# Performance work log

Measured on AMD Instinct MI355X. Metric: run time of the kernel, lower is better.

## Reference

```python
import jax, jax.numpy as jnp
import numpy as np

N_NODES = 100000
N_EDGES = 1000000
D_IN, H1, H2, D_OUT = 64, 64, 32, 16


def gcn_conv(x, W, b, src, dst, n):
    # PyG GCNConv: add self-loops, symmetric normalization deg^-1/2 A deg^-1/2, then linear.
    h = x @ W  # [N, out]
    ones = jnp.ones(src.shape[0], dtype=x.dtype)
    deg = jax.ops.segment_sum(ones, dst, num_segments=n) + 1.0  # +1 for self-loop
    dinv = jnp.where(deg > 0, jax.lax.rsqrt(deg), 0.0)
    coef = dinv[src] * dinv[dst]  # [E]
    msg = h[src] * coef[:, None]  # [E, out]
    agg = jax.ops.segment_sum(msg, dst, num_segments=n)
    agg = agg + h * (dinv * dinv)[:, None]  # self-loop contribution
    return agg + b


def setup_inputs() -> dict:
    key = jax.random.key(0)
    ks = jax.random.split(key, 16)
    s = 0.1
    inp = {
        "x": jax.random.normal(ks[0], (N_NODES, D_IN), jnp.float32),
        "edge_index": jax.random.randint(ks[1], (2, N_EDGES), 0, N_NODES, jnp.int64),
        # SELayer params
        "U_w": jax.random.normal(ks[2], (D_IN, D_IN), jnp.float32) * s,
        "U_b": jnp.zeros((D_IN,), jnp.float32),
        "fc1_w": jax.random.normal(ks[3], (D_IN, D_IN // 4), jnp.float32) * s,
        "fc1_b": jnp.zeros((D_IN // 4,), jnp.float32),
        "fc2_w": jax.random.normal(ks[4], (D_IN // 4, D_IN), jnp.float32) * s,
        "fc2_b": jnp.zeros((D_IN,), jnp.float32),
        # GCN layers
        "W1": jax.random.normal(ks[5], (D_IN, H1), jnp.float32) * s,
        "b1": jnp.zeros((H1,), jnp.float32),
        "W2": jax.random.normal(ks[6], (H1, H2), jnp.float32) * s,
        "b2": jnp.zeros((H2,), jnp.float32),
        # classifier
        "fc_w": jax.random.normal(ks[7], (H2, D_OUT), jnp.float32) * s,
        "fc_b": jnp.zeros((D_OUT,), jnp.float32),
    }
    return inp


def reference(x, edge_index, U_w, U_b, fc1_w, fc1_b, fc2_w, fc2_b, W1, b1, W2, b2, fc_w, fc_b):
    n = x.shape[0]
    src, dst = edge_index[0], edge_index[1]
    # SE layer
    xu = x @ U_w + U_b
    w = jax.nn.sigmoid(jax.nn.relu(xu @ fc1_w + fc1_b) @ fc2_w + fc2_b)
    h = xu * w
    # GCN stack (dropout is identity in eval mode)
    h = jax.nn.relu(gcn_conv(h, W1, b1, src, dst, n))
    h = jax.nn.relu(gcn_conv(h, W2, b2, src, dst, n))
    logits = h @ fc_w + fc_b
    return jax.nn.log_softmax(logits, axis=1), w
```

## Files before the change

kernel.cpp:

```cpp
#include <hip/hip_runtime.h>
#include <hip/hip_bf16.h>

#define NN 100000
#define NE 1000000
#define CAP 64
#define PADS 16

#define NPER 196
#define GRID_FAT (NPER * 13)

__device__ __forceinline__ float f4c(const float4& v, int i) {
    switch (i) { case 0: return v.x; case 1: return v.y; case 2: return v.z; default: return v.w; }
}
__device__ __forceinline__ unsigned short f2bf(float f) {
    unsigned u = __float_as_uint(f);
    return (unsigned short)((u + 0x7FFFu + ((u >> 16) & 1u)) >> 16);
}
__device__ __forceinline__ float bf2f(unsigned short s) {
    return __uint_as_float(((unsigned)s) << 16);
}

__global__ __launch_bounds__(256) void fat_kernel(
    const float* __restrict__ x, const void* __restrict__ eidx,
    const float* __restrict__ U_w, const float* __restrict__ U_b,
    const float* __restrict__ f1w, const float* __restrict__ f1b,
    const float* __restrict__ f2w, const float* __restrict__ f2b,
    const float* __restrict__ W1,
    int* __restrict__ cnt_pad, int* __restrict__ bucket,
    unsigned short* __restrict__ hW1b, float* __restrict__ w_out)
{
    const int b = blockIdx.x;
    const int r13 = b % 13;
    const int tid = threadIdx.x;

    if (r13 < 5) {
        const int sidx = (b / 13) * 5 + r13;
        long e0 = ((long)sidx * 256 + tid) * 4;
        if (e0 >= NE) return;

        const unsigned* pp = (const unsigned*)eidx;
        bool is64 = true;
#pragma unroll
        for (int k = 0; k < 8; ++k)
            if (pp[2 * k + 1] != 0u) is64 = false;

        int srcs[4], dsts[4];
        if (is64) {
            const long long* p = (const long long*)eidx;
#pragma unroll
            for (int i = 0; i < 4; ++i) {
                srcs[i] = (int)p[e0 + i];
                dsts[i] = (int)p[NE + e0 + i];
            }
        } else {
            const int* p = (const int*)eidx;
            int4 s4 = *(const int4*)&p[e0];
            int4 d4 = *(const int4*)&p[NE + e0];
            srcs[0] = s4.x; srcs[1] = s4.y; srcs[2] = s4.z; srcs[3] = s4.w;
            dsts[0] = d4.x; dsts[1] = d4.y; dsts[2] = d4.z; dsts[3] = d4.w;
        }

        int pos[4];
#pragma unroll
        for (int i = 0; i < 4; ++i) pos[i] = atomicAdd(&cnt_pad[dsts[i] * PADS], 1);
#pragma unroll
        for (int i = 0; i < 4; ++i)
            if (pos[i] < CAP) bucket[dsts[i] * CAP + pos[i]] = srcs[i];
        return;
    }

    const int seidx = (b / 13) * 8 + (r13 - 5);
    const long base = (long)seidx * 64;
    if (base >= NN) return;

    __shared__ float sU[64][68];
    __shared__ float sx[64][68];
    __shared__ float sF1[64 * 16];
    __shared__ float st1[64][20];
    __shared__ float sF2[16][68];
    __shared__ float sUb[64], sb1[16], sb2[64];

    for (int i = tid; i < 1024; i += 256) {
        int r = i >> 4, q = i & 15;
        *(float4*)&sU[r][q * 4] = *(const float4*)&U_w[r * 64 + q * 4];
    }
    for (int i = tid; i < 1024; i += 256) {
        int r = i >> 4, q = i & 15;
        long row = base + r;
        float4 v = make_float4(0.f, 0.f, 0.f, 0.f);
        if (row < NN) v = *(const float4*)&x[row * 64 + q * 4];
        *(float4*)&sx[r][q * 4] = v;
    }
    for (int i = tid; i < 1024; i += 256) sF1[i] = f1w[i];
    {
        int r = tid >> 4, q = tid & 15;
        *(float4*)&sF2[r][q * 4] = *(const float4*)&f2w[r * 64 + q * 4];
    }
    if (tid < 64) sUb[tid] = U_b[tid];
    if (tid < 16) sb1[tid] = f1b[tid];
    if (tid < 64) sb2[tid] = f2b[tid];
    __syncthreads();

    const int cg = tid & 15, rg = tid >> 4;
    const int r0 = rg * 4, c0 = cg * 4;

    float acc[4][4];
#pragma unroll
    for (int ri = 0; ri < 4; ++ri)
#pragma unroll
        for (int ci = 0; ci < 4; ++ci) acc[ri][ci] = 0.f;

#pragma unroll 4
    for (int kk = 0; kk < 64; kk += 4) {
        float4 xa[4];
#pragma unroll
        for (int ri = 0; ri < 4; ++ri) xa[ri] = *(float4*)&sx[r0 + ri][kk];
#pragma unroll
        for (int kq = 0; kq < 4; ++kq) {
            float4 ub = *(float4*)&sU[kk + kq][c0];
#pragma unroll
            for (int ri = 0; ri < 4; ++ri) {
                float xv = f4c(xa[ri], kq);
                acc[ri][0] = fmaf(xv, ub.x, acc[ri][0]);
                acc[ri][1] = fmaf(xv, ub.y, acc[ri][1]);
                acc[ri][2] = fmaf(xv, ub.z, acc[ri][2]);
                acc[ri][3] = fmaf(xv, ub.w, acc[ri][3]);
            }
        }
    }
    __syncthreads();

#pragma unroll
    for (int ri = 0; ri < 4; ++ri) {
        acc[ri][0] += sUb[c0 + 0];
        acc[ri][1] += sUb[c0 + 1];
        acc[ri][2] += sUb[c0 + 2];
        acc[ri][3] += sUb[c0 + 3];
        float4 o = make_float4(acc[ri][0], acc[ri][1], acc[ri][2], acc[ri][3]);
        *(float4*)&sx[r0 + ri][c0] = o;
    }
    __syncthreads();

    float a1[4] = {sb1[cg], sb1[cg], sb1[cg], sb1[cg]};
#pragma unroll 4
    for (int kk = 0; kk < 64; kk += 4) {
        float4 xa[4];
#pragma unroll
        for (int ri = 0; ri < 4; ++ri) xa[ri] = *(float4*)&sx[r0 + ri][kk];
#pragma unroll
        for (int kq = 0; kq < 4; ++kq) {
            float wv = sF1[(kk + kq) * 16 + cg];
#pragma unroll
            for (int ri = 0; ri < 4; ++ri) a1[ri] = fmaf(f4c(xa[ri], kq), wv, a1[ri]);
        }
    }
#pragma unroll
    for (int ri = 0; ri < 4; ++ri) st1[r0 + ri][cg] = fmaxf(a1[ri], 0.f);
    __syncthreads();

    float a2[4][4];
#pragma unroll
    for (int ri = 0; ri < 4; ++ri)
#pragma unroll
        for (int ci = 0; ci < 4; ++ci) a2[ri][ci] = sb2[c0 + ci];

#pragma unroll
    for (int kk = 0; kk < 16; kk += 4) {
        float4 ta[4];
#pragma unroll
        for (int ri = 0; ri < 4; ++ri) ta[ri] = *(float4*)&st1[r0 + ri][kk];
#pragma unroll
        for (int kq = 0; kq < 4; ++kq) {
            float4 fb = *(float4*)&sF2[kk + kq][c0];
#pragma unroll
            for (int ri = 0; ri < 4; ++ri) {
                float xv = f4c(ta[ri], kq);
                a2[ri][0] = fmaf(xv, fb.x, a2[ri][0]);
                a2[ri][1] = fmaf(xv, fb.y, a2[ri][1]);
                a2[ri][2] = fmaf(xv, fb.z, a2[ri][2]);
                a2[ri][3] = fmaf(xv, fb.w, a2[ri][3]);
            }
        }
    }
#pragma unroll
    for (int ri = 0; ri < 4; ++ri) {
        long row = base + r0 + ri;
        float4 wv;
        wv.x = 1.f / (1.f + expf(-a2[ri][0]));
        wv.y = 1.f / (1.f + expf(-a2[ri][1]));
        wv.z = 1.f / (1.f + expf(-a2[ri][2]));
        wv.w = 1.f / (1.f + expf(-a2[ri][3]));
        float4 h4;
        h4.x = acc[ri][0] * wv.x; h4.y = acc[ri][1] * wv.y;
        h4.z = acc[ri][2] * wv.z; h4.w = acc[ri][3] * wv.w;
        *(float4*)&sx[r0 + ri][c0] = h4;
        if (row < NN) *(float4*)&w_out[row * 64 + c0] = wv;
    }
    for (int i = tid; i < 1024; i += 256) {
        int r = i >> 4, q = i & 15;
        *(float4*)&sU[r][q * 4] = *(const float4*)&W1[r * 64 + q * 4];
    }
    __syncthreads();

#pragma unroll
    for (int ri = 0; ri < 4; ++ri)
#pragma unroll
        for (int ci = 0; ci < 4; ++ci) acc[ri][ci] = 0.f;

#pragma unroll 4
    for (int kk = 0; kk < 64; kk += 4) {
        float4 xa[4];
#pragma unroll
        for (int ri = 0; ri < 4; ++ri) xa[ri] = *(float4*)&sx[r0 + ri][kk];
#pragma unroll
        for (int kq = 0; kq < 4; ++kq) {
            float4 wb = *(float4*)&sU[kk + kq][c0];
#pragma unroll
            for (int ri = 0; ri < 4; ++ri) {
                float xv = f4c(xa[ri], kq);
                acc[ri][0] = fmaf(xv, wb.x, acc[ri][0]);
                acc[ri][1] = fmaf(xv, wb.y, acc[ri][1]);
                acc[ri][2] = fmaf(xv, wb.z, acc[ri][2]);
                acc[ri][3] = fmaf(xv, wb.w, acc[ri][3]);
            }
        }
    }
#pragma unroll
    for (int ri = 0; ri < 4; ++ri) {
        long row = base + r0 + ri;
        if (row < NN) {
            ushort4 o;
            o.x = f2bf(acc[ri][0]); o.y = f2bf(acc[ri][1]);
            o.z = f2bf(acc[ri][2]); o.w = f2bf(acc[ri][3]);
            *(ushort4*)&hW1b[(size_t)row * 64 + c0] = o;
        }
    }
}

__global__ __launch_bounds__(256) void dinv_k(const int* __restrict__ cnt_pad,
                                              int* __restrict__ cnt,
                                              float* __restrict__ dinv)
{
    long i = (long)blockIdx.x * 256 + threadIdx.x;
    if (i < NN) {
        int c = cnt_pad[i * PADS];
        dinv[i] = rsqrtf((float)c + 1.0f);
        cnt[i] = (c > CAP) ? CAP : c;
    }
}

__global__ __launch_bounds__(256) void gather64_fused(
    const int* __restrict__ cnt, const int* __restrict__ bucket,
    const float* __restrict__ dinv, const unsigned short* __restrict__ hW1b,
    const float* __restrict__ b1, const float* __restrict__ W2,
    unsigned short* __restrict__ hW2b)
{
    __shared__ float sW2[64 * 32];
    __shared__ float srow[4][64];

    const int tid = threadIdx.x;
    for (int i = tid; i < 512; i += 256)
        *(float4*)&sW2[i * 4] = *(const float4*)&W2[i * 4];

    const int w = tid >> 6;
    const int l = tid & 63;
    const int q = l >> 4;
    const int p = l & 15;
    const long row = (long)blockIdx.x * 4 + w;
    const bool valid = (row < NN);

    int deg = valid ? cnt[row] : 0;
    float dr = valid ? dinv[row] : 0.f;
    const int* bk = bucket + row * CAP;

    int   mysrc = (l < deg) ? bk[l] : 0;
    float mycf  = (l < deg) ? dinv[mysrc] * dr : 0.f;

    float4 acc = make_float4(0.f, 0.f, 0.f, 0.f);
#pragma unroll 2
    for (int e = 0; e < deg; e += 4) {
        int   src = __shfl(mysrc, e + q);
        float cf  = __shfl(mycf,  e + q);
        ushort4 v4 = *(const ushort4*)&hW1b[(size_t)src * 64 + p * 4];
        acc.x = fmaf(bf2f(v4.x), cf, acc.x);
        acc.y = fmaf(bf2f(v4.y), cf, acc.y);
        acc.z = fmaf(bf2f(v4.z), cf, acc.z);
        acc.w = fmaf(bf2f(v4.w), cf, acc.w);
    }
#pragma unroll
    for (int o = 16; o <= 32; o <<= 1) {
        acc.x += __shfl_xor(acc.x, o);
        acc.y += __shfl_xor(acc.y, o);
        acc.z += __shfl_xor(acc.z, o);
        acc.w += __shfl_xor(acc.w, o);
    }
    if (q == 0) {
        ushort4 h4 = valid ? *(const ushort4*)&hW1b[(size_t)row * 64 + p * 4]
                           : make_ushort4(0, 0, 0, 0);
        float4 bb = *(const float4*)&b1[p * 4];
        float dd = dr * dr;
        float4 a1;
        a1.x = fmaxf(fmaf(bf2f(h4.x), dd, bb.x) + acc.x, 0.f);
        a1.y = fmaxf(fmaf(bf2f(h4.y), dd, bb.y) + acc.y, 0.f);
        a1.z = fmaxf(fmaf(bf2f(h4.z), dd, bb.z) + acc.z, 0.f);
        a1.w = fmaxf(fmaf(bf2f(h4.w), dd, bb.w) + acc.w, 0.f);
        *(float4*)&srow[w][p * 4] = a1;
    }
    __syncthreads();

    const int c = l & 31, s = l >> 5;
    float acc2 = 0.f;
#pragma unroll
    for (int kk = 0; kk < 32; ++kk) {
        int k = s * 32 + kk;
        acc2 = fmaf(srow[w][k], sW2[k * 32 + c], acc2);
    }
    acc2 += __shfl_xor(acc2, 32);
    if (s == 0 && valid) hW2b[(size_t)row * 32 + c] = f2bf(acc2);
}

__global__ __launch_bounds__(256) void gather32_fused(
    const int* __restrict__ cnt, const int* __restrict__ bucket,
    const float* __restrict__ dinv, const unsigned short* __restrict__ hW2b,
    const float* __restrict__ b2, const float* __restrict__ fcw,
    const float* __restrict__ fcb, float* __restrict__ out)
{
    __shared__ float sfc[32 * 16];
    __shared__ float srow[4][40];

    const int tid = threadIdx.x;
    for (int i = tid; i < 128; i += 256)
        *(float4*)&sfc[i * 4] = *(const float4*)&fcw[i * 4];

    const int w = tid >> 6;
    const int l = tid & 63;
    const int q = l >> 3;
    const int p = l & 7;
    const long row = (long)blockIdx.x * 4 + w;
    const bool valid = (row < NN);

    int deg = valid ? cnt[row] : 0;
    float dr = valid ? dinv[row] : 0.f;
    const int* bk = bucket + row * CAP;

    int   mysrc = (l < deg) ? bk[l] : 0;
    float mycf  = (l < deg) ? dinv[mysrc] * dr : 0.f;

    float4 acc = make_float4(0.f, 0.f, 0.f, 0.f);
#pragma unroll 2
    for (int e = 0; e < deg; e += 8) {
        int   src = __shfl(mysrc, e + q);
        float cf  = __shfl(mycf,  e + q);
        ushort4 v4 = *(const ushort4*)&hW2b[(size_t)src * 32 + p * 4];
        acc.x = fmaf(bf2f(v4.x), cf, acc.x);
        acc.y = fmaf(bf2f(v4.y), cf, acc.y);
        acc.z = fmaf(bf2f(v4.z), cf, acc.z);
        acc.w = fmaf(bf2f(v4.w), cf, acc.w);
    }
#pragma unroll
    for (int o = 8; o <= 32; o <<= 1) {
        acc.x += __shfl_xor(acc.x, o);
        acc.y += __shfl_xor(acc.y, o);
        acc.z += __shfl_xor(acc.z, o);
        acc.w += __shfl_xor(acc.w, o);
    }
    if (q == 0) {
        ushort4 h4 = valid ? *(const ushort4*)&hW2b[(size_t)row * 32 + p * 4]
                           : make_ushort4(0, 0, 0, 0);
        float4 bb = *(const float4*)&b2[p * 4];
        float dd = dr * dr;
        float4 h2;
        h2.x = fmaxf(fmaf(bf2f(h4.x), dd, bb.x) + acc.x, 0.f);
        h2.y = fmaxf(fmaf(bf2f(h4.y), dd, bb.y) + acc.y, 0.f);
        h2.z = fmaxf(fmaf(bf2f(h4.z), dd, bb.z) + acc.z, 0.f);
        h2.w = fmaxf(fmaf(bf2f(h4.w), dd, bb.w) + acc.w, 0.f);
        *(float4*)&srow[w][p * 4] = h2;
    }
    __syncthreads();

    if (tid < 64) {
        const int r = tid >> 4, c = tid & 15;
        float lg = fcb[c];
#pragma unroll
        for (int k = 0; k < 32; ++k)
            lg = fmaf(srow[r][k], sfc[k * 16 + c], lg);
        float m = lg;
        for (int o = 8; o >= 1; o >>= 1) m = fmaxf(m, __shfl_xor(m, o, 16));
        float ex = expf(lg - m);
        float sum = ex;
        for (int o = 8; o >= 1; o >>= 1) sum += __shfl_xor(sum, o, 16);
        long orow = (long)blockIdx.x * 4 + r;
        if (orow < NN) out[orow * 16 + c] = lg - m - logf(sum);
    }
}

extern "C" void kernel_launch(void* const* d_in, const int* in_sizes, int n_in,
                              void* d_out, int out_size, void* d_ws, size_t ws_size,
                              hipStream_t stream)
{
    const float* x    = (const float*)d_in[0];
    const void*  eidx = d_in[1];
    const float* U_w  = (const float*)d_in[2];
    const float* U_b  = (const float*)d_in[3];
    const float* f1w  = (const float*)d_in[4];
    const float* f1b  = (const float*)d_in[5];
    const float* f2w  = (const float*)d_in[6];
    const float* f2b  = (const float*)d_in[7];
    const float* W1   = (const float*)d_in[8];
    const float* b1   = (const float*)d_in[9];
    const float* W2   = (const float*)d_in[10];
    const float* b2   = (const float*)d_in[11];
    const float* fcw  = (const float*)d_in[12];
    const float* fcb  = (const float*)d_in[13];

    float* out0 = (float*)d_out;
    float* wout = (float*)d_out + 1600000;

    float* ws = (float*)d_ws;

    int*            cnt     = (int*)ws;
    float*          dinv    = ws + 100000;
    int*            cnt_pad = (int*)(ws + 200000);
    int*            bucket  = (int*)(ws + 1800000);
    unsigned short* hW1b    = (unsigned short*)(ws + 8200000);
    unsigned short* hW2b    = (unsigned short*)(ws + 11400000);

    hipMemsetAsync(cnt_pad, 0, (size_t)NN * PADS * sizeof(int), stream);

    fat_kernel<<<GRID_FAT, 256, 0, stream>>>(x, eidx, U_w, U_b, f1w, f1b, f2w, f2b,
                                             W1, cnt_pad, bucket, hW1b, wout);
    dinv_k<<<(NN + 255) / 256, 256, 0, stream>>>(cnt_pad, cnt, dinv);

    gather64_fused<<<NN / 4, 256, 0, stream>>>(cnt, bucket, dinv, hW1b, b1, W2, hW2b);
    gather32_fused<<<NN / 4, 256, 0, stream>>>(cnt, bucket, dinv, hW2b, b2, fcw, fcb, out0);
}
```

Baseline: 180.0 us.

## Partition edge bucketing by destination range per XCD and read SE weights from global

The edge-bucketing blocks now each scan an 8000-edge chunk and handle only edges whose destination falls in one of eight 12500-node ranges chosen by blockIdx&7. The likely aim is to keep each range's counter atomics and bucket writes local to one XCD's L2. Every destination index is therefore read eight times, which adds read traffic and branch divergence. Separately, the SE block stops staging fc1/fc2 weights in shared memory and reads them directly from global, cutting LDS use and one staging step.

```diff
diff --git a/kernel.cpp b/kernel.cpp
--- a/kernel.cpp
+++ b/kernel.cpp
@@ -6,8 +6,11 @@
 #define CAP 64
 #define PADS 16
 
-#define NPER 196
-#define GRID_FAT (NPER * 13)
+#define SUPER 104
+#define NSP 25
+#define GRID_FAT (SUPER * NSP)
+#define RANGE_N 12500
+#define CHUNK_E 8000
 
 __device__ __forceinline__ float f4c(const float4& v, int i) {
     switch (i) { case 0: return v.x; case 1: return v.y; case 2: return v.z; default: return v.w; }
@@ -34,9 +37,11 @@
     const int tid = threadIdx.x;
 
     if (r13 < 5) {
-        const int sidx = (b / 13) * 5 + r13;
-        long e0 = ((long)sidx * 256 + tid) * 4;
-        if (e0 >= NE) return;
+        const int r8 = b & 7;
+        const int c  = (b / SUPER) * 5 + r13;
+        const long cb = (long)c * CHUNK_E;
+        const int lo = r8 * RANGE_N;
+        const int hi = lo + RANGE_N;
 
         const unsigned* pp = (const unsigned*)eidx;
         bool is64 = true;
@@ -44,28 +49,41 @@
         for (int k = 0; k < 8; ++k)
             if (pp[2 * k + 1] != 0u) is64 = false;
 
-        int srcs[4], dsts[4];
         if (is64) {
             const long long* p = (const long long*)eidx;
-#pragma unroll
-            for (int i = 0; i < 4; ++i) {
-                srcs[i] = (int)p[e0 + i];
-                dsts[i] = (int)p[NE + e0 + i];
+            const int* p32 = (const int*)eidx;
+#pragma unroll 2
+            for (int i = 0; i < 8; ++i) {
+                long e0 = cb + (long)i * 1024 + tid * 4;
+                int4 qa = *(const int4*)&p32[(NE + e0) * 2];
+                int4 qb = *(const int4*)&p32[(NE + e0) * 2 + 4];
+                int d[4] = {qa.x, qa.z, qb.x, qb.z};
+#pragma unroll
+                for (int j = 0; j < 4; ++j) {
+                    if (d[j] >= lo && d[j] < hi) {
+                        int src = (int)p[e0 + j];
+                        int pos = atomicAdd(&cnt_pad[d[j] * PADS], 1);
+                        if (pos < CAP) bucket[d[j] * CAP + pos] = src;
+                    }
+                }
             }
         } else {
             const int* p = (const int*)eidx;
-            int4 s4 = *(const int4*)&p[e0];
-            int4 d4 = *(const int4*)&p[NE + e0];
-            srcs[0] = s4.x; srcs[1] = s4.y; srcs[2] = s4.z; srcs[3] = s4.w;
-            dsts[0] = d4.x; dsts[1] = d4.y; dsts[2] = d4.z; dsts[3] = d4.w;
-        }
-
-        int pos[4];
-#pragma unroll
-        for (int i = 0; i < 4; ++i) pos[i] = atomicAdd(&cnt_pad[dsts[i] * PADS], 1);
-#pragma unroll
-        for (int i = 0; i < 4; ++i)
-            if (pos[i] < CAP) bucket[dsts[i] * CAP + pos[i]] = srcs[i];
+#pragma unroll 2
+            for (int i = 0; i < 8; ++i) {
+                long e0 = cb + (long)i * 1024 + tid * 4;
+                int4 d4 = *(const int4*)&p[NE + e0];
+                int d[4] = {d4.x, d4.y, d4.z, d4.w};
+#pragma unroll
+                for (int j = 0; j < 4; ++j) {
+                    if (d[j] >= lo && d[j] < hi) {
+                        int src = p[e0 + j];
+                        int pos = atomicAdd(&cnt_pad[d[j] * PADS], 1);
+                        if (pos < CAP) bucket[d[j] * CAP + pos] = src;
+                    }
+                }
+            }
+        }
         return;
     }
 
@@ -75,9 +93,7 @@
 
     __shared__ float sU[64][68];
     __shared__ float sx[64][68];
-    __shared__ float sF1[64 * 16];
     __shared__ float st1[64][20];
-    __shared__ float sF2[16][68];
     __shared__ float sUb[64], sb1[16], sb2[64];
 
     for (int i = tid; i < 1024; i += 256) {
@@ -90,11 +106,6 @@
         float4 v = make_float4(0.f, 0.f, 0.f, 0.f);
         if (row < NN) v = *(const float4*)&x[row * 64 + q * 4];
         *(float4*)&sx[r][q * 4] = v;
-    }
-    for (int i = tid; i < 1024; i += 256) sF1[i] = f1w[i];
-    {
-        int r = tid >> 4, q = tid & 15;
-        *(float4*)&sF2[r][q * 4] = *(const float4*)&f2w[r * 64 + q * 4];
     }
     if (tid < 64) sUb[tid] = U_b[tid];
     if (tid < 16) sb1[tid] = f1b[tid];
@@ -149,7 +160,7 @@
         for (int ri = 0; ri < 4; ++ri) xa[ri] = *(float4*)&sx[r0 + ri][kk];
 #pragma unroll
         for (int kq = 0; kq < 4; ++kq) {
-            float wv = sF1[(kk + kq) * 16 + cg];
+            float wv = f1w[(kk + kq) * 16 + cg];
 #pragma unroll
             for (int ri = 0; ri < 4; ++ri) a1[ri] = fmaf(f4c(xa[ri], kq), wv, a1[ri]);
         }
@@ -171,7 +182,7 @@
         for (int ri = 0; ri < 4; ++ri) ta[ri] = *(float4*)&st1[r0 + ri][kk];
 #pragma unroll
         for (int kq = 0; kq < 4; ++kq) {
-            float4 fb = *(float4*)&sF2[kk + kq][c0];
+            float4 fb = *(const float4*)&f2w[(kk + kq) * 64 + c0];
 #pragma unroll
             for (int ri = 0; ri < 4; ++ri) {
                 float xv = f4c(ta[ri], kq);
```

New measurement: 218.4 us. 1.21x slower.

## Store per-node edge counter inside bucket row and drop padded count array

Applied to the files above, without the earlier changes.

Moves each node's atomic edge counter into slot 0 of its 64-int bucket row, so the padded count array is gone and the 6.4MB memset becomes a small zeroing kernel. Counter and bucket entries now share a cache line, which should make the atomic and the scatter store touch the same line. Usable neighbor capacity drops from 64 to 63. Separately, the SE block no longer stages the fc1/fc2 weights in shared memory and reads them straight from global memory, trading LDS use for more global and cache traffic.

```diff
diff --git a/kernel.cpp b/kernel.cpp
--- a/kernel.cpp
+++ b/kernel.cpp
@@ -4,7 +4,6 @@
 #define NN 100000
 #define NE 1000000
 #define CAP 64
-#define PADS 16
 
 #define NPER 196
 #define GRID_FAT (NPER * 13)
@@ -18,6 +17,12 @@
 }
 __device__ __forceinline__ float bf2f(unsigned short s) {
     return __uint_as_float(((unsigned)s) << 16);
+}
+
+__global__ __launch_bounds__(256) void zero_k(int* __restrict__ bucket)
+{
+    long i = (long)blockIdx.x * 256 + threadIdx.x;
+    if (i < NN) bucket[i * CAP] = 0;
 }
 
 __global__ __launch_bounds__(256) void fat_kernel(
@@ -26,7 +31,7 @@
     const float* __restrict__ f1w, const float* __restrict__ f1b,
     const float* __restrict__ f2w, const float* __restrict__ f2b,
     const float* __restrict__ W1,
-    int* __restrict__ cnt_pad, int* __restrict__ bucket,
+    int* __restrict__ bucket,
     unsigned short* __restrict__ hW1b, float* __restrict__ w_out)
 {
     const int b = blockIdx.x;
@@ -62,10 +67,10 @@
 
         int pos[4];
 #pragma unroll
-        for (int i = 0; i < 4; ++i) pos[i] = atomicAdd(&cnt_pad[dsts[i] * PADS], 1);
+        for (int i = 0; i < 4; ++i) pos[i] = atomicAdd(&bucket[dsts[i] * CAP], 1);
 #pragma unroll
         for (int i = 0; i < 4; ++i)
-            if (pos[i] < CAP) bucket[dsts[i] * CAP + pos[i]] = srcs[i];
+            if (pos[i] < CAP - 1) bucket[dsts[i] * CAP + 1 + pos[i]] = srcs[i];
         return;
     }
 
@@ -75,9 +80,7 @@
 
     __shared__ float sU[64][68];
     __shared__ float sx[64][68];
-    __shared__ float sF1[64 * 16];
     __shared__ float st1[64][20];
-    __shared__ float sF2[16][68];
     __shared__ float sUb[64], sb1[16], sb2[64];
 
     for (int i = tid; i < 1024; i += 256) {
@@ -90,11 +93,6 @@
         float4 v = make_float4(0.f, 0.f, 0.f, 0.f);
         if (row < NN) v = *(const float4*)&x[row * 64 + q * 4];
         *(float4*)&sx[r][q * 4] = v;
-    }
-    for (int i = tid; i < 1024; i += 256) sF1[i] = f1w[i];
-    {
-        int r = tid >> 4, q = tid & 15;
-        *(float4*)&sF2[r][q * 4] = *(const float4*)&f2w[r * 64 + q * 4];
     }
     if (tid < 64) sUb[tid] = U_b[tid];
     if (tid < 16) sb1[tid] = f1b[tid];
@@ -149,7 +147,7 @@
         for (int ri = 0; ri < 4; ++ri) xa[ri] = *(float4*)&sx[r0 + ri][kk];
 #pragma unroll
         for (int kq = 0; kq < 4; ++kq) {
-            float wv = sF1[(kk + kq) * 16 + cg];
+            float wv = f1w[(kk + kq) * 16 + cg];
 #pragma unroll
             for (int ri = 0; ri < 4; ++ri) a1[ri] = fmaf(f4c(xa[ri], kq), wv, a1[ri]);
         }
@@ -171,7 +169,7 @@
         for (int ri = 0; ri < 4; ++ri) ta[ri] = *(float4*)&st1[r0 + ri][kk];
 #pragma unroll
         for (int kq = 0; kq < 4; ++kq) {
-            float4 fb = *(float4*)&sF2[kk + kq][c0];
+            float4 fb = *(const float4*)&f2w[(kk + kq) * 64 + c0];
 #pragma unroll
             for (int ri = 0; ri < 4; ++ri) {
                 float xv = f4c(ta[ri], kq);
@@ -237,15 +235,15 @@
     }
 }
 
-__global__ __launch_bounds__(256) void dinv_k(const int* __restrict__ cnt_pad,
+__global__ __launch_bounds__(256) void dinv_k(const int* __restrict__ bucket,
                                               int* __restrict__ cnt,
                                               float* __restrict__ dinv)
 {
     long i = (long)blockIdx.x * 256 + threadIdx.x;
     if (i < NN) {
-        int c = cnt_pad[i * PADS];
+        int c = bucket[i * CAP];
         dinv[i] = rsqrtf((float)c + 1.0f);
-        cnt[i] = (c > CAP) ? CAP : c;
+        cnt[i] = (c > CAP - 1) ? CAP - 1 : c;
     }
 }
 
@@ -271,7 +269,7 @@
 
     int deg = valid ? cnt[row] : 0;
     float dr = valid ? dinv[row] : 0.f;
-    const int* bk = bucket + row * CAP;
+    const int* bk = bucket + row * CAP + 1;
 
     int   mysrc = (l < deg) ? bk[l] : 0;
     float mycf  = (l < deg) ? dinv[mysrc] * dr : 0.f;
@@ -341,7 +339,7 @@
 
     int deg = valid ? cnt[row] : 0;
     float dr = valid ? dinv[row] : 0.f;
-    const int* bk = bucket + row * CAP;
+    const int* bk = bucket + row * CAP + 1;
 
     int   mysrc = (l < deg) ? bk[l] : 0;
     float mycf  = (l < deg) ? dinv[mysrc] * dr : 0.f;
@@ -420,16 +418,15 @@
 
     int*            cnt     = (int*)ws;
     float*          dinv    = ws + 100000;
-    int*            cnt_pad = (int*)(ws + 200000);
     int*            bucket  = (int*)(ws + 1800000);
     unsigned short* hW1b    = (unsigned short*)(ws + 8200000);
     unsigned short* hW2b    = (unsigned short*)(ws + 11400000);
 
-    hipMemsetAsync(cnt_pad, 0, (size_t)NN * PADS * sizeof(int), stream);
+    zero_k<<<(NN + 255) / 256, 256, 0, stream>>>(bucket);
 
     fat_kernel<<<GRID_FAT, 256, 0, stream>>>(x, eidx, U_w, U_b, f1w, f1b, f2w, f2b,
-                                             W1, cnt_pad, bucket, hW1b, wout);
-    dinv_k<<<(NN + 255) / 256, 256, 0, stream>>>(cnt_pad, cnt, dinv);
+                                             W1, bucket, hW1b, wout);
+    dinv_k<<<(NN + 255) / 256, 256, 0, stream>>>(bucket, cnt, dinv);
 
     gather64_fused<<<NN / 4, 256, 0, stream>>>(cnt, bucket, dinv, hW1b, b1, W2, hW2b);
     gather32_fused<<<NN / 4, 256, 0, stream>>>(cnt, bucket, dinv, hW2b, b2, fcw, fcb, out0);
```

New measurement: 182.0 us. No clear change (+1.1%).
